# Performance work log

Hardware: AMD Instinct MI355X
Metric: run time of the kernel (lower is better)

Reference implementation:

```python
import jax, jax.numpy as jnp
import numpy as np

HEADS = 8
DIM_HEAD = 64
MP_ADD_T = 0.3
EPS = 1e-4


def normalize_weight(w, eps=EPS):
    # Karras forced weight norm: per-output-channel L2 norm over all other dims
    dims = tuple(range(1, w.ndim))
    n = jnp.sqrt(jnp.sum(w * w, axis=dims, keepdims=True))
    alpha = np.sqrt(n.size / w.size)  # = 1/sqrt(fan_in)
    return w / (eps + alpha * n)


def pixel_norm(t, eps=EPS):
    # F.normalize(dim=-1) * sqrt(d): x / max(||x||, eps) * sqrt(d)
    n = jnp.sqrt(jnp.sum(t * t, axis=-1, keepdims=True))
    return t / jnp.maximum(n, eps) * np.sqrt(t.shape[-1])


def conv1x1(x, w):
    # x: [b,c,h,w], w: [o,c] (normalized weight / sqrt(fan_in))
    wn = normalize_weight(w) / np.sqrt(w.shape[1])  # fan_in = dim_in * 1 * 1
    return jnp.einsum('bchw,oc->bohw', x, wn)


def setup_inputs() -> dict:
    key = jax.random.key(0)
    k1, k2, k3, k4 = jax.random.split(key, 4)
    b, c, h, w = 16, 512, 32, 32
    hidden = HEADS * DIM_HEAD
    return {
        'x': jax.random.normal(k1, (b, c, h, w), dtype=jnp.float32),
        'w_qkv': jax.random.normal(k2, (hidden * 3, c), dtype=jnp.float32),
        'w_out': jax.random.normal(k3, (c, hidden), dtype=jnp.float32),
        'mem_kv': jax.random.normal(k4, (2, HEADS, 4, DIM_HEAD), dtype=jnp.float32),
    }


def reference(x, w_qkv, w_out, mem_kv):
    b, c, h, w = x.shape
    n = h * w
    qkv = conv1x1(x, w_qkv)  # [b, 3*hidden, h, w]
    q, k, v = jnp.split(qkv, 3, axis=1)

    def to_heads(t):
        # b (h c) x y -> b h (x y) c
        return t.reshape(b, HEADS, DIM_HEAD, n).transpose(0, 1, 3, 2)

    q, k, v = map(to_heads, (q, k, v))
    mk = jnp.broadcast_to(mem_kv[0], (b,) + mem_kv[0].shape)  # [b,h,m,d]
    mv = jnp.broadcast_to(mem_kv[1], (b,) + mem_kv[1].shape)
    k = jnp.concatenate([mk, k], axis=2)
    v = jnp.concatenate([mv, v], axis=2)

    q, k, v = map(pixel_norm, (q, k, v))

    sim = jnp.einsum('bhid,bhjd->bhij', q, k) * (DIM_HEAD ** -0.5)
    attn = jax.nn.softmax(sim, axis=-1)  # dropout is identity in eval
    out = jnp.einsum('bhij,bhjd->bhid', attn, v)  # [b,h,n,d]

    # b h (x y) d -> b (h d) x y
    out = out.transpose(0, 1, 3, 2).reshape(b, HEADS * DIM_HEAD, h, w)
    out = conv1x1(out, w_out)

    # MPAdd: magnitude-preserving residual
    t = MP_ADD_T
    den = np.sqrt((1 - t) ** 2 + t ** 2)
    return (out * (1.0 - t) + x * t) / den
```

## Files before the change

### kernel.cpp

```cpp
#include <hip/hip_runtime.h>
#include <hip/hip_bf16.h>
#include <math.h>

#define HEADS 8
#define DIMH 64
#define NPIX 1024
#define BATCH 16
#define CIN 512
#define HIDDEN 512
#define OQKV 1536

typedef __attribute__((ext_vector_type(8))) short v8s;
typedef __attribute__((ext_vector_type(4))) float v4f;
typedef __attribute__((ext_vector_type(4))) int v4i;

#define MFMA16(a, b, c) __builtin_amdgcn_mfma_f32_16x16x32_bf16(a, b, c, 0, 0, 0)

__device__ inline unsigned pkbf(float lo, float hi) {
    unsigned r;
    asm("v_cvt_pk_bf16_f32 %0, %1, %2" : "=v"(r) : "v"(lo), "v"(hi));
    return r;
}
__device__ inline ushort bf16u(float f) {
    __hip_bfloat16 h = __float2bfloat16(f);
    return *(ushort*)&h;
}
__device__ inline float exp2i(float x) {
    float r;
    asm("v_exp_f32 %0, %1" : "=v"(r) : "v"(x));
    return r;
}
__device__ inline void gload16(const ushort* g, ushort* l) {
    __builtin_amdgcn_global_load_lds(
        (const __attribute__((address_space(1))) void*)g,
        (__attribute__((address_space(3))) void*)l, 16, 0, 0);
}

#define INVLN2 1.44269504088896f
#define BIAS2  12.2629078475662f

__global__ __launch_bounds__(256) void prep_fused(
    const float* __restrict__ x,
    const float* __restrict__ wq, const float* __restrict__ wo,
    const float* __restrict__ mem_kv,
    ushort* __restrict__ Xt, ushort* __restrict__ wn,
    __hip_bfloat16* __restrict__ mk, __hip_bfloat16* __restrict__ mv,
    float* __restrict__ msk, float* __restrict__ msv)
{
    int bid = blockIdx.x;
    if (bid < 2048) {
        int b = bid >> 7, rem = bid & 127;
        int c0 = (rem >> 4) * 64, p0 = (rem & 15) * 64;
        __shared__ ushort lds[64][72];
        int tid = threadIdx.x;
        int cl = tid >> 2;
        int pl = (tid & 3) * 16;
        const float* src = x + ((size_t)b * CIN + c0 + cl) * NPIX + p0 + pl;
        #pragma unroll
        for (int j = 0; j < 4; j++) {
            float4 v = *(const float4*)(src + j * 4);
            lds[cl][pl + j * 4 + 0] = bf16u(v.x);
            lds[cl][pl + j * 4 + 1] = bf16u(v.y);
            lds[cl][pl + j * 4 + 2] = bf16u(v.z);
            lds[cl][pl + j * 4 + 3] = bf16u(v.w);
        }
        __syncthreads();
        int pw = tid >> 2;
        int cs = (tid & 3) * 16;
        union { ushort u[16]; uint4 q[2]; } tmp;
        #pragma unroll
        for (int j = 0; j < 16; j++) tmp.u[j] = lds[cs + j][pw];
        ushort* dst = Xt + ((size_t)b * NPIX + p0 + pw) * CIN + c0 + cs;
        *(uint4*)(dst) = tmp.q[0];
        *(uint4*)(dst + 8) = tmp.q[1];
    } else if (bid < 4096) {
        int row = bid - 2048;
        const float* src = (row < OQKV) ? (wq + (size_t)row * CIN)
                                        : (wo + (size_t)(row - OQKV) * CIN);
        int t = threadIdx.x;
        float v0 = src[t];
        float v1 = src[t + 256];
        float ss = v0 * v0 + v1 * v1;
        #pragma unroll
        for (int off = 32; off >= 1; off >>= 1) ss += __shfl_xor(ss, off);
        __shared__ float red[4];
        if ((t & 63) == 0) red[t >> 6] = ss;
        __syncthreads();
        float total = red[0] + red[1] + red[2] + red[3];
        const float RSQRT512 = 0.044194173824159216f;
        const float SQRT512  = 22.627416997969522f;
        float scale = 1.0f / ((1e-4f + sqrtf(total) * RSQRT512) * SQRT512);
        ushort* dst = wn + (size_t)row * CIN;
        dst[t] = bf16u(v0 * scale);
        dst[t + 256] = bf16u(v1 * scale);
    } else {
        if (threadIdx.x < 64) {
            int h = bid - 4096;
            int lane = threadIdx.x;
            #pragma unroll
            for (int m = 0; m < 4; m++) {
                float kvv = mem_kv[((size_t)h * 4 + m) * 64 + lane];
                float vvv = mem_kv[((size_t)(HEADS + h) * 4 + m) * 64 + lane];
                float ssk = kvv * kvv, ssv = vvv * vvv;
                #pragma unroll
                for (int off = 32; off >= 1; off >>= 1) {
                    ssk += __shfl_xor(ssk, off);
                    ssv += __shfl_xor(ssv, off);
                }
                float sck = 8.0f / fmaxf(sqrtf(ssk), 1e-4f);
                float scv = 8.0f / fmaxf(sqrtf(ssv), 1e-4f);
                mk[((size_t)h * 16 + m) * 64 + lane] = __float2bfloat16(kvv);
                mv[((size_t)h * 64 + lane) * 32 + m] = __float2bfloat16(vvv);
                if (lane == 0) { msk[h * 16 + m] = sck; msv[h * 32 + m] = scv; }
            }
            #pragma unroll
            for (int m = 4; m < 16; m++)
                mk[((size_t)h * 16 + m) * 64 + lane] = __float2bfloat16(0.f);
            #pragma unroll
            for (int m = 4; m < 32; m++)
                mv[((size_t)h * 64 + lane) * 32 + m] = __float2bfloat16(0.f);
            if (lane >= 4 && lane < 16) msk[h * 16 + lane] = 0.f;
            if (lane >= 4 && lane < 32) msv[h * 32 + lane] = 0.f;
        }
    }
}

__global__ __launch_bounds__(256) void gemm_qkv_mfma(
    const ushort* __restrict__ Wall,
    const ushort* __restrict__ Xt,
    ushort* __restrict__ Qb, ushort* __restrict__ Kb, ushort* __restrict__ Vb,
    float* __restrict__ qsA, float* __restrict__ ksA, float* __restrict__ vsA)
{
    int bid = blockIdx.x;
    int xcd = bid & 7;
    int rest = bid >> 3;
    int bh2 = rest / 96;
    int r = rest - bh2 * 96;
    int b = xcd + (bh2 << 3);
    int yy = r % 12;
    int pp = r / 12;

    int p0 = pp * 128;
    int isV = (yy >= 8) ? 1 : 0;
    int o0 = (isV ? (yy - 8) : yy) * 128;
    const ushort* Wsrc = Wall + (isV ? (size_t)1024 * CIN : 0);

    int tid = threadIdx.x;
    int wave = tid >> 6, lane = tid & 63;
    int wy = wave >> 1, wx = wave & 1;
    int col = lane & 15, lg = lane >> 4;
    int pw = p0 + wx * 64;
    int ow = o0 + wy * 64;

    __shared__ __align__(16) ushort sW[128 * 64];
    __shared__ __align__(16) ushort sX[128 * 64];

    int rIn = lane >> 3;
    int chS = (lane & 7) ^ rIn;
    int rowStage = wave * 32 + rIn;
    const ushort* gW = Wsrc + (size_t)(o0 + rowStage) * CIN + chS * 8;
    const ushort* gX = Xt + ((size_t)b * NPIX + p0 + rowStage) * CIN + chS * 8;

    v4f acc[4][4];
    #pragma unroll
    for (int i = 0; i < 4; i++)
        #pragma unroll
        for (int j = 0; j < 4; j++) acc[i][j] = (v4f){0.f, 0.f, 0.f, 0.f};

    const ushort* sA = isV ? sX : sW;
    const ushort* sB = isV ? sW : sX;
    int rowA = (isV ? wx : wy) * 64 + col;
    int rowB = (isV ? wy : wx) * 64 + col;
    int c7 = col & 7;

    #pragma unroll 1
    for (int c0 = 0; c0 < CIN; c0 += 64) {
        #pragma unroll
        for (int j = 0; j < 4; j++) {
            gload16(gW + (size_t)j * 8 * CIN + c0, &sW[(wave * 4 + j) * 512]);
            gload16(gX + (size_t)j * 8 * CIN + c0, &sX[(wave * 4 + j) * 512]);
        }
        __syncthreads();
        #pragma unroll
        for (int hh = 0; hh < 2; hh++) {
            int ch = (hh * 4 + lg) ^ c7;
            v8s af[4], bf[4];
            #pragma unroll
            for (int i = 0; i < 4; i++) {
                af[i] = *(const v8s*)&sA[(rowA + i * 16) * 64 + ch * 8];
                bf[i] = *(const v8s*)&sB[(rowB + i * 16) * 64 + ch * 8];
            }
            #pragma unroll
            for (int i = 0; i < 4; i++)
                #pragma unroll
                for (int j = 0; j < 4; j++)
                    acc[i][j] = MFMA16(af[i], bf[j], acc[i][j]);
        }
        __syncthreads();
    }

    if (!isV) {
        int part = ow >> 9;
        int h = (ow >> 6) & 7;
        int bh = b * HEADS + h;

        float ssq[4];
        #pragma unroll
        for (int pt = 0; pt < 4; pt++) {
            float s = 0.f;
            #pragma unroll
            for (int dt = 0; dt < 4; dt++)
                #pragma unroll
                for (int r2 = 0; r2 < 4; r2++) s += acc[dt][pt][r2] * acc[dt][pt][r2];
            s += __shfl_xor(s, 16);
            s += __shfl_xor(s, 32);
            ssq[pt] = s;
        }
        float num = part ? 8.0f : 1.0f;
        if (lg == 0) {
            float* sAr = part ? ksA : qsA;
            #pragma unroll
            for (int pt = 0; pt < 4; pt++)
                sAr[(size_t)bh * NPIX + pw + pt * 16 + col] =
                    num / fmaxf(sqrtf(ssq[pt]), 1e-4f);
        }
        ushort* dst = (part ? Kb : Qb) + (size_t)bh * NPIX * DIMH;
        #pragma unroll
        for (int pt = 0; pt < 4; pt++) {
            int p = pw + pt * 16 + col;
            #pragma unroll
            for (int dt = 0; dt < 4; dt++) {
                uint2 uu;
                uu.x = pkbf(acc[dt][pt][0], acc[dt][pt][1]);
                uu.y = pkbf(acc[dt][pt][2], acc[dt][pt][3]);
                *(uint2*)(dst + (size_t)p * DIMH + dt * 16 + 4 * lg) = uu;
            }
        }
    } else {
        int h = (ow >> 6) & 7;
        int bh = b * HEADS + h;

        #pragma unroll
        for (int pt = 0; pt < 4; pt++) {
            #pragma unroll
            for (int r2 = 0; r2 < 4; r2++) {
                float s = acc[pt][0][r2] * acc[pt][0][r2] + acc[pt][1][r2] * acc[pt][1][r2]
                        + acc[pt][2][r2] * acc[pt][2][r2] + acc[pt][3][r2] * acc[pt][3][r2];
                s += __shfl_xor(s, 1);
                s += __shfl_xor(s, 2);
                s += __shfl_xor(s, 4);
                s += __shfl_xor(s, 8);
                float sc = 8.0f / fmaxf(sqrtf(s), 1e-4f);
                if (col == 0)
                    vsA[(size_t)bh * NPIX + pw + pt * 16 + 4 * lg + r2] = sc;
            }
        }
        #pragma unroll
        for (int ot = 0; ot < 4; ot++) {
            int d = ot * 16 + col;
            #pragma unroll
            for (int pt = 0; pt < 4; pt++) {
                uint2 uu;
                uu.x = pkbf(acc[pt][ot][0], acc[pt][ot][1]);
                uu.y = pkbf(acc[pt][ot][2], acc[pt][ot][3]);
                *(uint2*)(Vb + ((size_t)bh * DIMH + d) * NPIX + pw + pt * 16 + 4 * lg) = uu;
            }
        }
    }
}

__global__ __launch_bounds__(256, 2) void attn_mfma_kernel(
    const __hip_bfloat16* __restrict__ Qb,
    const __hip_bfloat16* __restrict__ Kb,
    const __hip_bfloat16* __restrict__ Vb,
    const float* __restrict__ qsA, const float* __restrict__ ksA,
    const float* __restrict__ vsA,
    const __hip_bfloat16* __restrict__ mk, const __hip_bfloat16* __restrict__ mv,
    const float* __restrict__ msk, const float* __restrict__ msv,
    ushort* __restrict__ attT)
{
    int bid = blockIdx.x;
    int bh = bid & 127;
    int qb = bid >> 7;
    int b = bh >> 3, h = bh & 7;
    int wave = threadIdx.x >> 6, lane = threadIdx.x & 63;
    int col = lane & 15, lg = lane >> 4;
    int q0 = qb * 256 + wave * 64;

    __shared__ float sKs[NPIX], sVs[NPIX];
    {
        int t4 = threadIdx.x * 4;
        *(float4*)&sKs[t4] = *(const float4*)&ksA[(size_t)bh * NPIX + t4];
        *(float4*)&sVs[t4] = *(const float4*)&vsA[(size_t)bh * NPIX + t4];
    }
    __syncthreads();

    const __hip_bfloat16* Qbase = Qb + ((size_t)bh * NPIX + q0) * DIMH;
    const __hip_bfloat16* Kbase = Kb + (size_t)bh * NPIX * DIMH;
    const __hip_bfloat16* Vbase = Vb + (size_t)bh * DIMH * NPIX;

    v8s qf[4][2];
    float myqs[4];
    #pragma unroll
    for (int qt = 0; qt < 4; qt++) {
        #pragma unroll
        for (int dh = 0; dh < 2; dh++)
            qf[qt][dh] = *(const v8s*)(Qbase + (qt * 16 + col) * DIMH + dh * 32 + 8 * lg);
        myqs[qt] = qsA[(size_t)bh * NPIX + q0 + qt * 16 + col] * INVLN2;
    }

    v4f o_[4][4];
    #pragma unroll
    for (int qt = 0; qt < 4; qt++)
        #pragma unroll
        for (int dt = 0; dt < 4; dt++) o_[qt][dt] = (v4f){0.f, 0.f, 0.f, 0.f};
    float l_[4] = {0.f, 0.f, 0.f, 0.f};

    int srcA = ((lg & 1) << 5) + col;
    int srcB = srcA + 16;
    bool hig = (lg >= 2);

    {
        const __hip_bfloat16* mkh = mk + (size_t)h * 16 * DIMH;
        v8s kf0 = *(const v8s*)(mkh + col * DIMH + 8 * lg);
        v8s kf1 = *(const v8s*)(mkh + col * DIMH + 32 + 8 * lg);
        v8s vfm[4];
        #pragma unroll
        for (int dt = 0; dt < 4; dt++)
            vfm[dt] = *(const v8s*)(mv + ((size_t)h * DIMH + dt * 16 + col) * 32 + 8 * lg);
        float4 ksm = *(const float4*)&msk[h * 16 + 4 * lg];
        float4 vsm = *(const float4*)&msv[h * 32 + 4 * lg];
        float ksr[4] = {ksm.x, ksm.y, ksm.z, ksm.w};
        float vsr[4] = {vsm.x, vsm.y, vsm.z, vsm.w};

        #pragma unroll
        for (int qt = 0; qt < 4; qt++) {
            v4f c0 = (v4f){0.f, 0.f, 0.f, 0.f};
            c0 = MFMA16(kf0, qf[qt][0], c0);
            c0 = MFMA16(kf1, qf[qt][1], c0);
            float p0[4];
            #pragma unroll
            for (int r = 0; r < 4; r++) {
                float t = __builtin_fmaf(c0[r], myqs[qt] * ksr[r], -BIAS2);
                p0[r] = (lg == 0) ? exp2i(t) : 0.f;
                l_[qt] += p0[r];
            }
            unsigned A0 = pkbf(p0[0] * vsr[0], p0[1] * vsr[1]);
            unsigned A1 = pkbf(p0[2] * vsr[2], p0[3] * vsr[3]);
            int a0 = __shfl((int)A0, srcA), a1 = __shfl((int)A1, srcA);
            int a2 = __shfl((int)A0, srcB), a3 = __shfl((int)A1, srcB);
            v4i w;
            w.x = hig ? 0 : a0; w.y = hig ? 0 : a1;
            w.z = hig ? 0 : a2; w.w = hig ? 0 : a3;
            v8s pf = __builtin_bit_cast(v8s, w);
            #pragma unroll
            for (int dt = 0; dt < 4; dt++)
                o_[qt][dt] = MFMA16(vfm[dt], pf, o_[qt][dt]);
        }
    }

    v8s kfA[4], vfA[4], kfB[4], vfB[4];

    #define LOADK(dst, kk) { \
        const __hip_bfloat16* Kr = Kbase + (size_t)(kk) * DIMH; \
        dst[0] = *(const v8s*)(Kr + col * DIMH + 8 * lg); \
        dst[1] = *(const v8s*)(Kr + col * DIMH + 32 + 8 * lg); \
        dst[2] = *(const v8s*)(Kr + (16 + col) * DIMH + 8 * lg); \
        dst[3] = *(const v8s*)(Kr + (16 + col) * DIMH + 32 + 8 * lg); }
    #define LOADV(dst, kk) { \
        _Pragma("unroll") \
        for (int dt = 0; dt < 4; dt++) \
            dst[dt] = *(const v8s*)(Vbase + (size_t)(dt * 16 + col) * NPIX + (kk) + 8 * lg); }

    #define COMPUTE(kf, vf, kk) { \
        float4 ks0 = *(const float4*)&sKs[(kk) + 4 * lg]; \
        float4 ks1 = *(const float4*)&sKs[(kk) + 16 + 4 * lg]; \
        float4 vs0 = *(const float4*)&sVs[(kk) + 4 * lg]; \
        float4 vs1 = *(const float4*)&sVs[(kk) + 16 + 4 * lg]; \
        float ksr0[4] = {ks0.x, ks0.y, ks0.z, ks0.w}; \
        float ksr1[4] = {ks1.x, ks1.y, ks1.z, ks1.w}; \
        float vsr0[4] = {vs0.x, vs0.y, vs0.z, vs0.w}; \
        float vsr1[4] = {vs1.x, vs1.y, vs1.z, vs1.w}; \
        _Pragma("unroll") \
        for (int qt = 0; qt < 4; qt++) { \
            v4f c0 = (v4f){0.f, 0.f, 0.f, 0.f}; \
            v4f c1 = (v4f){0.f, 0.f, 0.f, 0.f}; \
            c0 = MFMA16(kf[0], qf[qt][0], c0); \
            c0 = MFMA16(kf[1], qf[qt][1], c0); \
            c1 = MFMA16(kf[2], qf[qt][0], c1); \
            c1 = MFMA16(kf[3], qf[qt][1], c1); \
            float p0[4], p1[4]; \
            _Pragma("unroll") \
            for (int r = 0; r < 4; r++) { \
                p0[r] = exp2i(__builtin_fmaf(c0[r], myqs[qt] * ksr0[r], -BIAS2)); \
                p1[r] = exp2i(__builtin_fmaf(c1[r], myqs[qt] * ksr1[r], -BIAS2)); \
                l_[qt] += p0[r] + p1[r]; \
            } \
            unsigned A0 = pkbf(p0[0] * vsr0[0], p0[1] * vsr0[1]); \
            unsigned A1 = pkbf(p0[2] * vsr0[2], p0[3] * vsr0[3]); \
            unsigned B0 = pkbf(p1[0] * vsr1[0], p1[1] * vsr1[1]); \
            unsigned B1 = pkbf(p1[2] * vsr1[2], p1[3] * vsr1[3]); \
            int a0 = __shfl((int)A0, srcA), a1 = __shfl((int)A1, srcA); \
            int a2 = __shfl((int)A0, srcB), a3 = __shfl((int)A1, srcB); \
            int b0 = __shfl((int)B0, srcA), b1 = __shfl((int)B1, srcA); \
            int b2 = __shfl((int)B0, srcB), b3 = __shfl((int)B1, srcB); \
            v4i w; \
            w.x = hig ? b0 : a0; w.y = hig ? b1 : a1; \
            w.z = hig ? b2 : a2; w.w = hig ? b3 : a3; \
            v8s pf = __builtin_bit_cast(v8s, w); \
            _Pragma("unroll") \
            for (int dt = 0; dt < 4; dt++) \
                o_[qt][dt] = MFMA16(vf[dt], pf, o_[qt][dt]); \
        } }

    LOADK(kfA, 0);
    LOADV(vfA, 0);
    #pragma unroll 1
    for (int k0 = 0; k0 < NPIX; k0 += 64) {
        LOADK(kfB, k0 + 32);
        LOADV(vfB, k0 + 32);
        COMPUTE(kfA, vfA, k0);
        LOADK(kfA, k0 + 64);
        LOADV(vfA, k0 + 64);
        COMPUTE(kfB, vfB, k0 + 32);
    }

    #pragma unroll
    for (int qt = 0; qt < 4; qt++) {
        float l = l_[qt];
        l += __shfl_xor(l, 16);
        l += __shfl_xor(l, 32);
        float invl = 1.0f / l;
        ushort* at = attT + ((size_t)(b * NPIX + q0 + qt * 16 + col)) * HIDDEN + h * DIMH;
        #pragma unroll
        for (int dt = 0; dt < 4; dt++) {
            uint2 uu;
            uu.x = pkbf(o_[qt][dt][0] * invl, o_[qt][dt][1] * invl);
            uu.y = pkbf(o_[qt][dt][2] * invl, o_[qt][dt][3] * invl);
            *(uint2*)(at + dt * 16 + 4 * lg) = uu;
        }
    }
    #undef LOADK
    #undef LOADV
    #undef COMPUTE
}

__global__ __launch_bounds__(256) void gemm_out_mfma(
    const ushort* __restrict__ Wo,
    const ushort* __restrict__ attT,
    const float* __restrict__ x, float* __restrict__ out)
{
    int b = blockIdx.z;
    int o0 = blockIdx.y * 128;
    int p0 = blockIdx.x * 128;
    int wave = threadIdx.x >> 6, lane = threadIdx.x & 63;
    int wy = wave >> 1, wx = wave & 1;
    int col = lane & 15, lg = lane >> 4;
    int ow = o0 + wy * 64, pw = p0 + wx * 64;

    const ushort* Abase = attT + ((size_t)b * NPIX + pw + col) * HIDDEN + 8 * lg;
    const ushort* Bbase = Wo + (size_t)(ow + col) * HIDDEN + 8 * lg;

    v4f acc[4][4];
    #pragma unroll
    for (int i = 0; i < 4; i++)
        #pragma unroll
        for (int j = 0; j < 4; j++) acc[i][j] = (v4f){0.f, 0.f, 0.f, 0.f};

    v8s a0[4], b0[4], a1[4], b1[4];
    #pragma unroll
    for (int i = 0; i < 4; i++) {
        a0[i] = *(const v8s*)(Abase + (size_t)i * 16 * HIDDEN);
        b0[i] = *(const v8s*)(Bbase + (size_t)i * 16 * HIDDEN);
    }
    #pragma unroll 1
    for (int c0 = 0; c0 < HIDDEN; c0 += 64) {
        #pragma unroll
        for (int i = 0; i < 4; i++) {
            a1[i] = *(const v8s*)(Abase + (size_t)i * 16 * HIDDEN + c0 + 32);
            b1[i] = *(const v8s*)(Bbase + (size_t)i * 16 * HIDDEN + c0 + 32);
        }
        #pragma unroll
        for (int pt = 0; pt < 4; pt++)
            #pragma unroll
            for (int ot = 0; ot < 4; ot++)
                acc[pt][ot] = MFMA16(a0[pt], b0[ot], acc[pt][ot]);
        if (c0 + 64 < HIDDEN) {
            #pragma unroll
            for (int i = 0; i < 4; i++) {
                a0[i] = *(const v8s*)(Abase + (size_t)i * 16 * HIDDEN + c0 + 64);
                b0[i] = *(const v8s*)(Bbase + (size_t)i * 16 * HIDDEN + c0 + 64);
            }
        }
        #pragma unroll
        for (int pt = 0; pt < 4; pt++)
            #pragma unroll
            for (int ot = 0; ot < 4; ot++)
                acc[pt][ot] = MFMA16(a1[pt], b1[ot], acc[pt][ot]);
    }

    const float INV_DEN = 1.3130643285972254f;
    #pragma unroll
    for (int pt = 0; pt < 4; pt++) {
        #pragma unroll
        for (int ot = 0; ot < 4; ot++) {
            size_t base = ((size_t)b * HIDDEN + ow + ot * 16 + col) * NPIX
                        + pw + pt * 16 + 4 * lg;
            float4 res = *(const float4*)&x[base];
            float4 y;
            y.x = (acc[pt][ot][0] * 0.7f + res.x * 0.3f) * INV_DEN;
            y.y = (acc[pt][ot][1] * 0.7f + res.y * 0.3f) * INV_DEN;
            y.z = (acc[pt][ot][2] * 0.7f + res.z * 0.3f) * INV_DEN;
            y.w = (acc[pt][ot][3] * 0.7f + res.w * 0.3f) * INV_DEN;
            *(float4*)&out[base] = y;
        }
    }
}

extern "C" void kernel_launch(void* const* d_in, const int* in_sizes, int n_in,
                              void* d_out, int out_size, void* d_ws, size_t ws_size,
                              hipStream_t stream)
{
    const float* x      = (const float*)d_in[0];
    const float* w_qkv  = (const float*)d_in[1];
    const float* w_out  = (const float*)d_in[2];
    const float* mem_kv = (const float*)d_in[3];
    float* out = (float*)d_out;

    char* ws = (char*)d_ws;
    ushort* wnB = (ushort*)ws; ws += (size_t)2048 * CIN * 2;
    ushort* Xt  = (ushort*)ws; ws += (size_t)BATCH * NPIX * CIN * 2;
    ushort* Qb  = (ushort*)ws; ws += (size_t)BATCH * HEADS * NPIX * DIMH * 2;
    ushort* Kb  = (ushort*)ws; ws += (size_t)BATCH * HEADS * NPIX * DIMH * 2;
    ushort* Vb  = (ushort*)ws; ws += (size_t)BATCH * HEADS * NPIX * DIMH * 2;
    ushort* attT = (ushort*)ws; ws += (size_t)BATCH * NPIX * HIDDEN * 2;
    float* qsA = (float*)ws;  ws += (size_t)BATCH * HEADS * NPIX * 4;
    float* ksA = (float*)ws;  ws += (size_t)BATCH * HEADS * NPIX * 4;
    float* vsA = (float*)ws;  ws += (size_t)BATCH * HEADS * NPIX * 4;
    float* msk = (float*)ws;  ws += 8 * 16 * 4;
    float* msv = (float*)ws;  ws += 8 * 32 * 4;
    __hip_bfloat16* mk = (__hip_bfloat16*)ws; ws += (size_t)8 * 16 * 64 * 2;
    __hip_bfloat16* mv = (__hip_bfloat16*)ws; ws += (size_t)8 * 64 * 32 * 2;

    prep_fused<<<4104, 256, 0, stream>>>(
        x, w_qkv, w_out, mem_kv, Xt, wnB, mk, mv, msk, msv);

    gemm_qkv_mfma<<<1536, 256, 0, stream>>>(
        wnB, Xt, Qb, Kb, Vb, qsA, ksA, vsA);

    attn_mfma_kernel<<<512, 256, 0, stream>>>(
        (const __hip_bfloat16*)Qb, (const __hip_bfloat16*)Kb,
        (const __hip_bfloat16*)Vb, qsA, ksA, vsA, mk, mv, msk, msv, attT);

    gemm_out_mfma<<<dim3(8, 4, BATCH), 256, 0, stream>>>(
        wnB + (size_t)OQKV * CIN, attT, x, out);
}
```

Measured before the change: 176.1 us.

## Fold V pixel-norm into V store, add MFMA priority, stage out-GEMM via LDS

The per-pixel V normalization scale is now applied when V is written in the QKV GEMM (and to memory values in prep), so the attention kernel no longer loads or multiplies by V scales and frees that shared buffer. The attention inner loop wraps its MFMA groups in s_setprio to favour matrix issue. The output projection GEMM now stages A and B tiles into swizzled LDS with global_load_lds instead of loading fragments directly from global memory per wave. These cut per-element multiplies and scale traffic and improve operand reuse, at the cost of extra barriers in the out-GEMM and no double buffering there.

```diff
diff --git a/kernel.cpp b/kernel.cpp
--- a/kernel.cpp
+++ b/kernel.cpp
@@ -45,7 +45,7 @@
     const float* __restrict__ mem_kv,
     ushort* __restrict__ Xt, ushort* __restrict__ wn,
     __hip_bfloat16* __restrict__ mk, __hip_bfloat16* __restrict__ mv,
-    float* __restrict__ msk, float* __restrict__ msv)
+    float* __restrict__ msk)
 {
     int bid = blockIdx.x;
     if (bid < 2048) {
@@ -110,8 +110,8 @@
                 float sck = 8.0f / fmaxf(sqrtf(ssk), 1e-4f);
                 float scv = 8.0f / fmaxf(sqrtf(ssv), 1e-4f);
                 mk[((size_t)h * 16 + m) * 64 + lane] = __float2bfloat16(kvv);
-                mv[((size_t)h * 64 + lane) * 32 + m] = __float2bfloat16(vvv);
-                if (lane == 0) { msk[h * 16 + m] = sck; msv[h * 32 + m] = scv; }
+                mv[((size_t)h * 64 + lane) * 32 + m] = __float2bfloat16(vvv * scv);
+                if (lane == 0) { msk[h * 16 + m] = sck; }
             }
             #pragma unroll
             for (int m = 4; m < 16; m++)
@@ -120,7 +120,6 @@
             for (int m = 4; m < 32; m++)
                 mv[((size_t)h * 64 + lane) * 32 + m] = __float2bfloat16(0.f);
             if (lane >= 4 && lane < 16) msk[h * 16 + lane] = 0.f;
-            if (lane >= 4 && lane < 32) msv[h * 32 + lane] = 0.f;
         }
     }
 }
@@ -129,7 +128,7 @@
     const ushort* __restrict__ Wall,
     const ushort* __restrict__ Xt,
     ushort* __restrict__ Qb, ushort* __restrict__ Kb, ushort* __restrict__ Vb,
-    float* __restrict__ qsA, float* __restrict__ ksA, float* __restrict__ vsA)
+    float* __restrict__ qsA, float* __restrict__ ksA)
 {
     int bid = blockIdx.x;
     int xcd = bid & 7;
@@ -240,6 +239,7 @@
         int h = (ow >> 6) & 7;
         int bh = b * HEADS + h;
 
+        float scl[4][4];
         #pragma unroll
         for (int pt = 0; pt < 4; pt++) {
             #pragma unroll
@@ -250,9 +250,7 @@
                 s += __shfl_xor(s, 2);
                 s += __shfl_xor(s, 4);
                 s += __shfl_xor(s, 8);
-                float sc = 8.0f / fmaxf(sqrtf(s), 1e-4f);
-                if (col == 0)
-                    vsA[(size_t)bh * NPIX + pw + pt * 16 + 4 * lg + r2] = sc;
+                scl[pt][r2] = 8.0f / fmaxf(sqrtf(s), 1e-4f);
             }
         }
         #pragma unroll
@@ -261,8 +259,8 @@
             #pragma unroll
             for (int pt = 0; pt < 4; pt++) {
                 uint2 uu;
-                uu.x = pkbf(acc[pt][ot][0], acc[pt][ot][1]);
-                uu.y = pkbf(acc[pt][ot][2], acc[pt][ot][3]);
+                uu.x = pkbf(acc[pt][ot][0] * scl[pt][0], acc[pt][ot][1] * scl[pt][1]);
+                uu.y = pkbf(acc[pt][ot][2] * scl[pt][2], acc[pt][ot][3] * scl[pt][3]);
                 *(uint2*)(Vb + ((size_t)bh * DIMH + d) * NPIX + pw + pt * 16 + 4 * lg) = uu;
             }
         }
@@ -274,9 +272,8 @@
     const __hip_bfloat16* __restrict__ Kb,
     const __hip_bfloat16* __restrict__ Vb,
     const float* __restrict__ qsA, const float* __restrict__ ksA,
-    const float* __restrict__ vsA,
     const __hip_bfloat16* __restrict__ mk, const __hip_bfloat16* __restrict__ mv,
-    const float* __restrict__ msk, const float* __restrict__ msv,
+    const float* __restrict__ msk,
     ushort* __restrict__ attT)
 {
     int bid = blockIdx.x;
@@ -287,11 +284,10 @@
     int col = lane & 15, lg = lane >> 4;
     int q0 = qb * 256 + wave * 64;
 
-    __shared__ float sKs[NPIX], sVs[NPIX];
+    __shared__ float sKs[NPIX];
     {
         int t4 = threadIdx.x * 4;
         *(float4*)&sKs[t4] = *(const float4*)&ksA[(size_t)bh * NPIX + t4];
-        *(float4*)&sVs[t4] = *(const float4*)&vsA[(size_t)bh * NPIX + t4];
     }
     __syncthreads();
 
@@ -329,9 +325,7 @@
         for (int dt = 0; dt < 4; dt++)
             vfm[dt] = *(const v8s*)(mv + ((size_t)h * DIMH + dt * 16 + col) * 32 + 8 * lg);
         float4 ksm = *(const float4*)&msk[h * 16 + 4 * lg];
-        float4 vsm = *(const float4*)&msv[h * 32 + 4 * lg];
         float ksr[4] = {ksm.x, ksm.y, ksm.z, ksm.w};
-        float vsr[4] = {vsm.x, vsm.y, vsm.z, vsm.w};
 
         #pragma unroll
         for (int qt = 0; qt < 4; qt++) {
@@ -345,8 +339,8 @@
                 p0[r] = (lg == 0) ? exp2i(t) : 0.f;
                 l_[qt] += p0[r];
             }
-            unsigned A0 = pkbf(p0[0] * vsr[0], p0[1] * vsr[1]);
-            unsigned A1 = pkbf(p0[2] * vsr[2], p0[3] * vsr[3]);
+            unsigned A0 = pkbf(p0[0], p0[1]);
+            unsigned A1 = pkbf(p0[2], p0[3]);
             int a0 = __shfl((int)A0, srcA), a1 = __shfl((int)A1, srcA);
             int a2 = __shfl((int)A0, srcB), a3 = __shfl((int)A1, srcB);
             v4i w;
@@ -375,20 +369,18 @@
     #define COMPUTE(kf, vf, kk) { \
         float4 ks0 = *(const float4*)&sKs[(kk) + 4 * lg]; \
         float4 ks1 = *(const float4*)&sKs[(kk) + 16 + 4 * lg]; \
-        float4 vs0 = *(const float4*)&sVs[(kk) + 4 * lg]; \
-        float4 vs1 = *(const float4*)&sVs[(kk) + 16 + 4 * lg]; \
         float ksr0[4] = {ks0.x, ks0.y, ks0.z, ks0.w}; \
         float ksr1[4] = {ks1.x, ks1.y, ks1.z, ks1.w}; \
-        float vsr0[4] = {vs0.x, vs0.y, vs0.z, vs0.w}; \
-        float vsr1[4] = {vs1.x, vs1.y, vs1.z, vs1.w}; \
         _Pragma("unroll") \
         for (int qt = 0; qt < 4; qt++) { \
             v4f c0 = (v4f){0.f, 0.f, 0.f, 0.f}; \
             v4f c1 = (v4f){0.f, 0.f, 0.f, 0.f}; \
+            __builtin_amdgcn_s_setprio(1); \
             c0 = MFMA16(kf[0], qf[qt][0], c0); \
             c0 = MFMA16(kf[1], qf[qt][1], c0); \
             c1 = MFMA16(kf[2], qf[qt][0], c1); \
             c1 = MFMA16(kf[3], qf[qt][1], c1); \
+            __builtin_amdgcn_s_setprio(0); \
             float p0[4], p1[4]; \
             _Pragma("unroll") \
             for (int r = 0; r < 4; r++) { \
@@ -396,10 +388,10 @@
                 p1[r] = exp2i(__builtin_fmaf(c1[r], myqs[qt] * ksr1[r], -BIAS2)); \
                 l_[qt] += p0[r] + p1[r]; \
             } \
-            unsigned A0 = pkbf(p0[0] * vsr0[0], p0[1] * vsr0[1]); \
-            unsigned A1 = pkbf(p0[2] * vsr0[2], p0[3] * vsr0[3]); \
-            unsigned B0 = pkbf(p1[0] * vsr1[0], p1[1] * vsr1[1]); \
-            unsigned B1 = pkbf(p1[2] * vsr1[2], p1[3] * vsr1[3]); \
+            unsigned A0 = pkbf(p0[0], p0[1]); \
+            unsigned A1 = pkbf(p0[2], p0[3]); \
+            unsigned B0 = pkbf(p1[0], p1[1]); \
+            unsigned B1 = pkbf(p1[2], p1[3]); \
             int a0 = __shfl((int)A0, srcA), a1 = __shfl((int)A1, srcA); \
             int a2 = __shfl((int)A0, srcB), a3 = __shfl((int)A1, srcB); \
             int b0 = __shfl((int)B0, srcA), b1 = __shfl((int)B1, srcA); \
@@ -408,9 +400,11 @@
             w.x = hig ? b0 : a0; w.y = hig ? b1 : a1; \
             w.z = hig ? b2 : a2; w.w = hig ? b3 : a3; \
             v8s pf = __builtin_bit_cast(v8s, w); \
+            __builtin_amdgcn_s_setprio(1); \
             _Pragma("unroll") \
             for (int dt = 0; dt < 4; dt++) \
                 o_[qt][dt] = MFMA16(vf[dt], pf, o_[qt][dt]); \
+            __builtin_amdgcn_s_setprio(0); \
         } }
 
     LOADK(kfA, 0);
@@ -453,13 +447,20 @@
     int b = blockIdx.z;
     int o0 = blockIdx.y * 128;
     int p0 = blockIdx.x * 128;
-    int wave = threadIdx.x >> 6, lane = threadIdx.x & 63;
+    int tid = threadIdx.x;
+    int wave = tid >> 6, lane = tid & 63;
     int wy = wave >> 1, wx = wave & 1;
     int col = lane & 15, lg = lane >> 4;
     int ow = o0 + wy * 64, pw = p0 + wx * 64;
 
-    const ushort* Abase = attT + ((size_t)b * NPIX + pw + col) * HIDDEN + 8 * lg;
-    const ushort* Bbase = Wo + (size_t)(ow + col) * HIDDEN + 8 * lg;
+    __shared__ __align__(16) ushort sAa[128 * 64];
+    __shared__ __align__(16) ushort sBb[128 * 64];
+
+    int rIn = lane >> 3;
+    int chS = (lane & 7) ^ rIn;
+    int rowStage = wave * 32 + rIn;
+    const ushort* gA = attT + ((size_t)b * NPIX + p0 + rowStage) * HIDDEN + chS * 8;
+    const ushort* gB = Wo + (size_t)(o0 + rowStage) * HIDDEN + chS * 8;
 
     v4f acc[4][4];
     #pragma unroll
@@ -467,36 +468,34 @@
         #pragma unroll
         for (int j = 0; j < 4; j++) acc[i][j] = (v4f){0.f, 0.f, 0.f, 0.f};
 
-    v8s a0[4], b0[4], a1[4], b1[4];
-    #pragma unroll
-    for (int i = 0; i < 4; i++) {
-        a0[i] = *(const v8s*)(Abase + (size_t)i * 16 * HIDDEN);
-        b0[i] = *(const v8s*)(Bbase + (size_t)i * 16 * HIDDEN);
-    }
+    int rowA = wx * 64 + col;
+    int rowB = wy * 64 + col;
+    int c7 = col & 7;
+
     #pragma unroll 1
     for (int c0 = 0; c0 < HIDDEN; c0 += 64) {
         #pragma unroll
-        for (int i = 0; i < 4; i++) {
-            a1[i] = *(const v8s*)(Abase + (size_t)i * 16 * HIDDEN + c0 + 32);
-            b1[i] = *(const v8s*)(Bbase + (size_t)i * 16 * HIDDEN + c0 + 32);
-        }
-        #pragma unroll
-        for (int pt = 0; pt < 4; pt++)
-            #pragma unroll
-            for (int ot = 0; ot < 4; ot++)
-                acc[pt][ot] = MFMA16(a0[pt], b0[ot], acc[pt][ot]);
-        if (c0 + 64 < HIDDEN) {
+        for (int j = 0; j < 4; j++) {
+            gload16(gA + (size_t)j * 8 * HIDDEN + c0, &sAa[(wave * 4 + j) * 512]);
+            gload16(gB + (size_t)j * 8 * HIDDEN + c0, &sBb[(wave * 4 + j) * 512]);
+        }
+        __syncthreads();
+        #pragma unroll
+        for (int hh = 0; hh < 2; hh++) {
+            int ch = (hh * 4 + lg) ^ c7;
+            v8s af[4], bf[4];
             #pragma unroll
             for (int i = 0; i < 4; i++) {
-                a0[i] = *(const v8s*)(Abase + (size_t)i * 16 * HIDDEN + c0 + 64);
-                b0[i] = *(const v8s*)(Bbase + (size_t)i * 16 * HIDDEN + c0 + 64);
-            }
-        }
-        #pragma unroll
-        for (int pt = 0; pt < 4; pt++)
-            #pragma unroll
-            for (int ot = 0; ot < 4; ot++)
-                acc[pt][ot] = MFMA16(a1[pt], b1[ot], acc[pt][ot]);
+                af[i] = *(const v8s*)&sAa[(rowA + i * 16) * 64 + ch * 8];
+                bf[i] = *(const v8s*)&sBb[(rowB + i * 16) * 64 + ch * 8];
+            }
+            #pragma unroll
+            for (int i = 0; i < 4; i++)
+                #pragma unroll
+                for (int j = 0; j < 4; j++)
+                    acc[i][j] = MFMA16(af[i], bf[j], acc[i][j]);
+        }
+        __syncthreads();
     }
 
     const float INV_DEN = 1.3130643285972254f;
@@ -536,21 +535,19 @@
     ushort* attT = (ushort*)ws; ws += (size_t)BATCH * NPIX * HIDDEN * 2;
     float* qsA = (float*)ws;  ws += (size_t)BATCH * HEADS * NPIX * 4;
     float* ksA = (float*)ws;  ws += (size_t)BATCH * HEADS * NPIX * 4;
-    float* vsA = (float*)ws;  ws += (size_t)BATCH * HEADS * NPIX * 4;
     float* msk = (float*)ws;  ws += 8 * 16 * 4;
-    float* msv = (float*)ws;  ws += 8 * 32 * 4;
     __hip_bfloat16* mk = (__hip_bfloat16*)ws; ws += (size_t)8 * 16 * 64 * 2;
     __hip_bfloat16* mv = (__hip_bfloat16*)ws; ws += (size_t)8 * 64 * 32 * 2;
 
     prep_fused<<<4104, 256, 0, stream>>>(
-        x, w_qkv, w_out, mem_kv, Xt, wnB, mk, mv, msk, msv);
+        x, w_qkv, w_out, mem_kv, Xt, wnB, mk, mv, msk);
 
     gemm_qkv_mfma<<<1536, 256, 0, stream>>>(
-        wnB, Xt, Qb, Kb, Vb, qsA, ksA, vsA);
+        wnB, Xt, Qb, Kb, Vb, qsA, ksA);
 
     attn_mfma_kernel<<<512, 256, 0, stream>>>(
         (const __hip_bfloat16*)Qb, (const __hip_bfloat16*)Kb,
-        (const __hip_bfloat16*)Vb, qsA, ksA, vsA, mk, mv, msk, msv, attT);
+        (const __hip_bfloat16*)Vb, qsA, ksA, mk, mv, msk, attT);
 
     gemm_out_mfma<<<dim3(8, 4, BATCH), 256, 0, stream>>>(
         wnB + (size_t)OQKV * CIN, attT, x, out);
```

Result: faster. 155.4 us (-11.8%).
